# Optimization experiments

Measured on AMD Instinct MI355X. Metric: run time of the kernel, lower is better.

## Reference

```python
import jax, jax.numpy as jnp
import numpy as np

ALPHA = 0.5
EPS = 1e-6
N = 16777216  # 2^24 rounds, ~64 MB per fp32 tensor


def setup_inputs() -> dict:
    key = jax.random.key(0)
    k1, k2 = jax.random.split(key)
    y_pred = jax.random.uniform(k1, (1, N), dtype=jnp.float32)
    y_true = jax.random.randint(k2, (1, N), 0, 2).astype(jnp.float32)
    # depth weights ((i+1)/N)**beta with beta = 1.0, as in compute_loss_for_scenario
    depth_weights = ((jnp.arange(N, dtype=jnp.float32) + 1.0) / N)[None, :]
    return {"y_pred": y_pred, "y_true": y_true, "depth_weights": depth_weights}


def reference(y_pred, y_true, depth_weights):
    # ---- weighted BCE ----
    log_p = jnp.log(y_pred + EPS)
    log_1mp = jnp.log(1.0 - y_pred + EPS)
    bce = -(y_true * log_p + (1.0 - y_true) * log_1mp)
    wbce = jnp.mean(depth_weights * bce)

    # ---- continuity-weighted loss (longest correct streak), vectorized ----
    n = y_true.shape[1]
    y_pred_bin = (y_pred > 0.5).astype(y_true.dtype)
    correct = (y_pred_bin == y_true).astype(jnp.float32)[0]  # [N]
    s = jnp.cumsum(correct)                                   # running count of corrects
    # at each failure, record the running count; cummax gives count at last failure
    reset_count = jnp.where(correct == 0.0, s, 0.0)
    last_reset = jax.lax.cummax(reset_count)
    streaks = s - last_reset                                  # current streak length at each i
    max_streak = jnp.max(streaks)
    cwl = 1.0 - max_streak / n

    return ALPHA * wbce + (1.0 - ALPHA) * cwl
```

## Files before the change

kernel.cpp:

```cpp
#include <hip/hip_runtime.h>


#define N_TOTAL 16777216
#define ITERS 16
#define ELEMS_PER_BLOCK (256 * 4 * ITERS)
#define NUM_BLOCKS (N_TOTAL / ELEMS_PER_BLOCK)
#define INV_N (1.0f / 16777216.0f)

struct Run { int pre, suf, mx, len; };

__device__ __forceinline__ Run run_combine(const Run& a, const Run& b) {
    Run r;
    r.mx  = max(max(a.mx, b.mx), a.suf + b.pre);
    r.pre = (a.pre == a.len) ? a.len + b.pre : a.pre;
    r.suf = (b.suf == b.len) ? b.len + a.suf : b.suf;
    r.len = a.len + b.len;
    return r;
}

__device__ __forceinline__ Run run_shfl_xor(const Run& a, int m) {
    Run r;
    r.pre = __shfl_xor(a.pre, m);
    r.suf = __shfl_xor(a.suf, m);
    r.mx  = __shfl_xor(a.mx, m);
    r.len = a.len;
    return r;
}

__device__ __forceinline__ Run run_wave_reduce(Run r, int lane) {
    #pragma unroll
    for (int m = 1; m < 64; m <<= 1) {
        Run o = run_shfl_xor(r, m);
        r = (lane & m) ? run_combine(o, r) : run_combine(r, o);
    }
    return r;
}

#define PRE_TAB 0x4010201030102010ull
#define SUF_TAB 0x4322111100000000ull
#define MAX_TAB 0x4322211132112110ull

__global__ __launch_bounds__(256) void stage1(const float* __restrict__ yp,
                                              const float* __restrict__ yt,
                                              int4* __restrict__ ws_run) {
    const int b = blockIdx.x, tid = threadIdx.x;
    const int wave = tid >> 6, lane = tid & 63;
    const float4* yp4 = (const float4*)yp;
    const float4* yt4 = (const float4*)yt;

    const int wave_start = (b * 4 + wave) * (ITERS * 256);

    float acc = 0.0f;
    Run wr = {0, 0, 0, 0};

    for (int j = 0; j < ITERS; ++j) {
        const int base_e = wave_start + j * 256;
        const int v = (base_e >> 2) + lane;
        float4 p4 = yp4[v];
        float4 t4 = yt4[v];
        float pa[4] = {p4.x, p4.y, p4.z, p4.w};
        float ta[4] = {t4.x, t4.y, t4.z, t4.w};

        unsigned msk = 0;
        #pragma unroll
        for (int k = 0; k < 4; ++k) {
            float p = pa[k], t = ta[k];
            bool tt = t > 0.5f;
            bool pb = p > 0.5f;
            float arg = tt ? (p + 1e-6f) : ((1.0f - p) + 1e-6f);
            float bce = -__logf(arg);
            float w = (float)(base_e + 4 * lane + k + 1) * INV_N;
            acc = fmaf(w, bce, acc);
            msk |= (unsigned)(pb == tt) << k;
        }

        Run ir;
        ir.pre = (int)((PRE_TAB >> (msk * 4)) & 0xF);
        ir.suf = (int)((SUF_TAB >> (msk * 4)) & 0xF);
        ir.mx  = (int)((MAX_TAB >> (msk * 4)) & 0xF);
        ir.len = 4;

        ir = run_wave_reduce(ir, lane);
        wr = run_combine(wr, ir);
    }

    #pragma unroll
    for (int m = 1; m < 64; m <<= 1) acc += __shfl_xor(acc, m);

    __shared__ Run wruns[4];
    __shared__ float wsum[4];
    if (lane == 0) { wruns[wave] = wr; wsum[wave] = acc; }
    __syncthreads();
    if (tid == 0) {
        Run r = wruns[0];
        float s = wsum[0];
        #pragma unroll
        for (int i = 1; i < 4; ++i) { r = run_combine(r, wruns[i]); s += wsum[i]; }
        ws_run[b] = make_int4(r.pre, r.suf, r.mx, __float_as_int(s));
    }
}

__global__ __launch_bounds__(256) void stage2(const int4* __restrict__ ws_run,
                                              float* __restrict__ out) {
    const int tid = threadIdx.x, wave = tid >> 6, lane = tid & 63;

    Run r = {0, 0, 0, 0};
    float s = 0.0f;
    #pragma unroll
    for (int i = 0; i < 4; ++i) {
        int4 v = ws_run[tid * 4 + i];
        Run q = {v.x, v.y, v.z, ELEMS_PER_BLOCK};
        r = run_combine(r, q);
        s += __int_as_float(v.w);
    }
    #pragma unroll
    for (int m = 1; m < 64; m <<= 1) {
        Run o = run_shfl_xor(r, m);
        r = (lane & m) ? run_combine(o, r) : run_combine(r, o);
        s += __shfl_xor(s, m);
    }

    __shared__ Run wruns[4];
    __shared__ float wsum[4];
    if (lane == 0) { wruns[wave] = r; wsum[wave] = s; }
    __syncthreads();
    if (tid == 0) {
        Run R = wruns[0];
        float S = wsum[0];
        #pragma unroll
        for (int i = 1; i < 4; ++i) { R = run_combine(R, wruns[i]); S += wsum[i]; }
        float wbce = S * INV_N;
        float cwl = 1.0f - (float)R.mx * INV_N;
        out[0] = 0.5f * wbce + 0.5f * cwl;
    }
}

extern "C" void kernel_launch(void* const* d_in, const int* in_sizes, int n_in,
                              void* d_out, int out_size, void* d_ws, size_t ws_size,
                              hipStream_t stream) {
    const float* yp = (const float*)d_in[0];
    const float* yt = (const float*)d_in[1];
    int4* ws_run = (int4*)d_ws;
    stage1<<<NUM_BLOCKS, 256, 0, stream>>>(yp, yt, ws_run);
    stage2<<<1, 256, 0, stream>>>(ws_run, (float*)d_out);
}
```

Baseline: 176.2 us.

## Replace per-iteration wave run scans with bit-mask transpose and single reduction

Instead of running a 6-step wave shuffle reduction of run triples for every iteration, each lane packs its 16×4 correctness bits into a 64-bit mask. A shuffle-based bit transpose then makes each lane hold 64 consecutive elements, and pre/suf/max runs come from ctz/clz and a log-step AND trick, followed by one wave reduction. The BCE argument becomes branchless FMA arithmetic, the weight scaling by 1/N is moved to the final stage, and the loop is fully unrolled with occupancy hints. This is meant to cut the shuffle- and ALU-heavy work per element, so the bandwidth-bound kernel approaches memory speed, at the cost of more complex bit manipulation and higher register pressure.

```diff
diff --git a/kernel.cpp b/kernel.cpp
--- a/kernel.cpp
+++ b/kernel.cpp
@@ -1,4 +1,5 @@
 #include <hip/hip_runtime.h>
+#include <stdint.h>
 
 
 #define N_TOTAL 16777216
@@ -18,85 +19,113 @@
     return r;
 }
 
-__device__ __forceinline__ Run run_shfl_xor(const Run& a, int m) {
-    Run r;
-    r.pre = __shfl_xor(a.pre, m);
-    r.suf = __shfl_xor(a.suf, m);
-    r.mx  = __shfl_xor(a.mx, m);
-    r.len = a.len;
-    return r;
+__device__ __forceinline__ unsigned long long shfl_xor_u64(unsigned long long x, int m) {
+    unsigned lo = (unsigned)__shfl_xor((int)(x & 0xFFFFFFFFull), m);
+    unsigned hi = (unsigned)__shfl_xor((int)(x >> 32), m);
+    return ((unsigned long long)hi << 32) | lo;
+}
+__device__ __forceinline__ unsigned long long shfl_u64(unsigned long long x, int src) {
+    unsigned lo = (unsigned)__shfl((int)(x & 0xFFFFFFFFull), src);
+    unsigned hi = (unsigned)__shfl((int)(x >> 32), src);
+    return ((unsigned long long)hi << 32) | lo;
 }
 
-__device__ __forceinline__ Run run_wave_reduce(Run r, int lane) {
-    #pragma unroll
-    for (int m = 1; m < 64; m <<= 1) {
-        Run o = run_shfl_xor(r, m);
-        r = (lane & m) ? run_combine(o, r) : run_combine(r, o);
-    }
-    return r;
+__device__ __forceinline__ unsigned long long bit_transpose(unsigned long long x, int lane) {
+    unsigned long long p;
+    const unsigned long long M2 = 0xF0F0F0F0F0F0F0F0ull;
+    p = shfl_xor_u64(x, 1);
+    x = (lane & 1) ? ((x & M2) | ((p >> 4) & ~M2)) : ((x & ~M2) | ((p << 4) & M2));
+    const unsigned long long M3 = 0xFF00FF00FF00FF00ull;
+    p = shfl_xor_u64(x, 2);
+    x = (lane & 2) ? ((x & M3) | ((p >> 8) & ~M3)) : ((x & ~M3) | ((p << 8) & M3));
+    const unsigned long long M4 = 0xFFFF0000FFFF0000ull;
+    p = shfl_xor_u64(x, 4);
+    x = (lane & 4) ? ((x & M4) | ((p >> 16) & ~M4)) : ((x & ~M4) | ((p << 16) & M4));
+    const unsigned long long M5 = 0xFFFFFFFF00000000ull;
+    p = shfl_xor_u64(x, 8);
+    x = (lane & 8) ? ((x & M5) | ((p >> 32) & ~M5)) : ((x & ~M5) | ((p << 32) & M5));
+    return x;
 }
 
-#define PRE_TAB 0x4010201030102010ull
-#define SUF_TAB 0x4322111100000000ull
-#define MAX_TAB 0x4322211132112110ull
-
-__global__ __launch_bounds__(256) void stage1(const float* __restrict__ yp,
-                                              const float* __restrict__ yt,
-                                              int4* __restrict__ ws_run) {
+__global__ __launch_bounds__(256, 4) void stage1(const float* __restrict__ yp,
+                                                 const float* __restrict__ yt,
+                                                 int4* __restrict__ ws_run) {
     const int b = blockIdx.x, tid = threadIdx.x;
     const int wave = tid >> 6, lane = tid & 63;
     const float4* yp4 = (const float4*)yp;
     const float4* yt4 = (const float4*)yt;
 
     const int wave_start = (b * 4 + wave) * (ITERS * 256);
+    const int v_base = (wave_start >> 2) + lane;
 
     float acc = 0.0f;
-    Run wr = {0, 0, 0, 0};
+    unsigned long long m64 = 0ull;
 
+    #pragma unroll
     for (int j = 0; j < ITERS; ++j) {
-        const int base_e = wave_start + j * 256;
-        const int v = (base_e >> 2) + lane;
+        const int v = v_base + j * 64;
         float4 p4 = yp4[v];
         float4 t4 = yt4[v];
         float pa[4] = {p4.x, p4.y, p4.z, p4.w};
         float ta[4] = {t4.x, t4.y, t4.z, t4.w};
+        const float fb = (float)(wave_start + j * 256 + 4 * lane + 1);
 
         unsigned msk = 0;
         #pragma unroll
         for (int k = 0; k < 4; ++k) {
             float p = pa[k], t = ta[k];
-            bool tt = t > 0.5f;
-            bool pb = p > 0.5f;
-            float arg = tt ? (p + 1e-6f) : ((1.0f - p) + 1e-6f);
-            float bce = -__logf(arg);
-            float w = (float)(base_e + 4 * lane + k + 1) * INV_N;
-            acc = fmaf(w, bce, acc);
-            msk |= (unsigned)(pb == tt) << k;
+            float u  = fmaf(2.0f, p, -1.0f);
+            float s0 = (1.0f + 1e-6f) - p;
+            float arg = fmaf(t, u, s0);
+            float lg = __logf(arg);
+            acc = fmaf(fb + (float)k, -lg, acc);
+            bool c = (p > 0.5f) == (t > 0.5f);
+            msk |= (unsigned)c << k;
         }
-
-        Run ir;
-        ir.pre = (int)((PRE_TAB >> (msk * 4)) & 0xF);
-        ir.suf = (int)((SUF_TAB >> (msk * 4)) & 0xF);
-        ir.mx  = (int)((MAX_TAB >> (msk * 4)) & 0xF);
-        ir.len = 4;
-
-        ir = run_wave_reduce(ir, lane);
-        wr = run_combine(wr, ir);
+        m64 |= (unsigned long long)msk << (4 * j);
     }
 
+    unsigned long long tm = bit_transpose(m64, lane);
+    const int src = ((lane & 3) << 4) | (lane >> 2);
+    tm = shfl_u64(tm, src);
+
+    unsigned long long nm = ~tm;
+    int pre = nm ? __builtin_ctzll(nm) : 64;
+    int suf = nm ? __builtin_clzll(nm) : 64;
+    int mx = 0;
+    {
+        unsigned long long y = tm, t2;
+        t2 = y & (y >> 32); if (t2) { mx += 32; y = t2; }
+        t2 = y & (y >> 16); if (t2) { mx += 16; y = t2; }
+        t2 = y & (y >> 8);  if (t2) { mx += 8;  y = t2; }
+        t2 = y & (y >> 4);  if (t2) { mx += 4;  y = t2; }
+        t2 = y & (y >> 2);  if (t2) { mx += 2;  y = t2; }
+        t2 = y & (y >> 1);  if (t2) { mx += 1;  y = t2; }
+        if (y) mx += 1;
+    }
+
+    Run r = {pre, suf, mx, 64};
     #pragma unroll
-    for (int m = 1; m < 64; m <<= 1) acc += __shfl_xor(acc, m);
+    for (int m = 1; m < 64; m <<= 1) {
+        Run o;
+        o.pre = __shfl_xor(r.pre, m);
+        o.suf = __shfl_xor(r.suf, m);
+        o.mx  = __shfl_xor(r.mx, m);
+        o.len = r.len;
+        r = (lane & m) ? run_combine(o, r) : run_combine(r, o);
+        acc += __shfl_xor(acc, m);
+    }
 
     __shared__ Run wruns[4];
     __shared__ float wsum[4];
-    if (lane == 0) { wruns[wave] = wr; wsum[wave] = acc; }
+    if (lane == 0) { wruns[wave] = r; wsum[wave] = acc; }
     __syncthreads();
     if (tid == 0) {
-        Run r = wruns[0];
+        Run R = wruns[0];
         float s = wsum[0];
         #pragma unroll
-        for (int i = 1; i < 4; ++i) { r = run_combine(r, wruns[i]); s += wsum[i]; }
-        ws_run[b] = make_int4(r.pre, r.suf, r.mx, __float_as_int(s));
+        for (int i = 1; i < 4; ++i) { R = run_combine(R, wruns[i]); s += wsum[i]; }
+        ws_run[b] = make_int4(R.pre, R.suf, R.mx, __float_as_int(s));
     }
 }
 
@@ -115,7 +144,11 @@
     }
     #pragma unroll
     for (int m = 1; m < 64; m <<= 1) {
-        Run o = run_shfl_xor(r, m);
+        Run o;
+        o.pre = __shfl_xor(r.pre, m);
+        o.suf = __shfl_xor(r.suf, m);
+        o.mx  = __shfl_xor(r.mx, m);
+        o.len = r.len;
         r = (lane & m) ? run_combine(o, r) : run_combine(r, o);
         s += __shfl_xor(s, m);
     }
@@ -129,7 +162,7 @@
         float S = wsum[0];
         #pragma unroll
         for (int i = 1; i < 4; ++i) { R = run_combine(R, wruns[i]); S += wsum[i]; }
-        float wbce = S * INV_N;
+        float wbce = S * INV_N * INV_N;
         float cwl = 1.0f - (float)R.mx * INV_N;
         out[0] = 0.5f * wbce + 0.5f * cwl;
     }
```

New measurement: 196.8 us. 11.7% more time.
